# Performance work log

Hardware: AMD Instinct MI355X
Metric: run time of the kernel (lower is better)

The kernel has to match this reference:

```python
import jax, jax.numpy as jnp
import numpy as np

B, S, D_IN = 2, 2048, 1024
H, DH = 16, 64          # num_heads, hidden_size (per-head dim)
D_MODEL = H * DH        # 1024
D_OUT = DH * 8          # 512


def setup_inputs() -> dict:
    key = jax.random.key(0)
    ks = jax.random.split(key, 9)
    s_in = 1.0 / np.sqrt(D_IN)
    s_md = 1.0 / np.sqrt(D_MODEL)
    return {
        "x": jax.random.normal(ks[0], (B, S, D_IN), dtype=jnp.float32),
        "Wq": jax.random.uniform(ks[1], (D_IN, D_MODEL), jnp.float32, -s_in, s_in),
        "bq": jax.random.uniform(ks[2], (D_MODEL,), jnp.float32, -s_in, s_in),
        "Wk": jax.random.uniform(ks[3], (D_IN, D_MODEL), jnp.float32, -s_in, s_in),
        "bk": jax.random.uniform(ks[4], (D_MODEL,), jnp.float32, -s_in, s_in),
        "Wv": jax.random.uniform(ks[5], (D_IN, D_MODEL), jnp.float32, -s_in, s_in),
        "bv": jax.random.uniform(ks[6], (D_MODEL,), jnp.float32, -s_in, s_in),
        "Wo": jax.random.uniform(ks[7], (D_MODEL, D_OUT), jnp.float32, -s_md, s_md),
        "bo": jax.random.uniform(ks[8], (D_OUT,), jnp.float32, -s_md, s_md),
    }


def reference(x, Wq, bq, Wk, bk, Wv, bv, Wo, bo):
    b, s, _ = x.shape
    # QKV projections -> [B, H, S, DH]
    def proj(W, bias):
        y = jnp.einsum("bsd,de->bse", x, W) + bias
        return y.reshape(b, s, H, DH).transpose(0, 2, 1, 3)
    Q, K, V = proj(Wq, bq), proj(Wk, bk), proj(Wv, bv)
    scores = jnp.einsum("bhqd,bhkd->bhqk", Q, K) / jnp.sqrt(jnp.float32(DH))
    weights = jax.nn.softmax(scores, axis=-1)
    attn = jnp.einsum("bhqk,bhkd->bhqd", weights, V)  # [B, H, S, DH]
    attn = attn.transpose(0, 2, 1, 3).reshape(b, s, H * DH)
    return jnp.einsum("bsd,de->bse", attn, Wo) + bo
```

## Files before the change

kernel.cpp:

```cpp
#include <hip/hip_runtime.h>

typedef __attribute__((ext_vector_type(8))) __bf16 bf16x8;
typedef __attribute__((ext_vector_type(4))) __bf16 bf16x4;
typedef __attribute__((ext_vector_type(4))) float f32x4;

#define MFMA16x16x32(A, B, C) __builtin_amdgcn_mfma_f32_16x16x32_bf16(A, B, C, 0, 0, 0)

__device__ __forceinline__ unsigned short f2bf(float f) {
    unsigned int u = __float_as_uint(f);
    u += 0x7fffu + ((u >> 16) & 1u);
    return (unsigned short)(u >> 16);
}

__device__ __forceinline__ unsigned cvtpk_bf16(float lo, float hi) {
    unsigned r;
    asm("v_cvt_pk_bf16_f32 %0, %1, %2" : "=v"(r) : "v"(lo), "v"(hi));
    return r;
}

__device__ __forceinline__ float exp2_hw(float x) {
    float r;
    asm("v_exp_f32 %0, %1" : "=v"(r) : "v"(x));
    return r;
}

__device__ __forceinline__ void gload16(const void* src, void* lds) {
    __builtin_amdgcn_global_load_lds(
        (const __attribute__((address_space(1))) unsigned int*)src,
        (__attribute__((address_space(3))) unsigned int*)lds,
        16, 0, 0);
}

__global__ __launch_bounds__(256) void cvt_x_kernel(const float* __restrict__ x,
                                                    unsigned short* __restrict__ xb) {
    const int i = (blockIdx.x * 256 + threadIdx.x) * 4;
    const float4 v = *(const float4*)(x + i);
    ushort4 o;
    o.x = f2bf(v.x); o.y = f2bf(v.y); o.z = f2bf(v.z); o.w = f2bf(v.w);
    *(ushort4*)(xb + i) = o;
}

__global__ __launch_bounds__(256) void tr_w_kernel(const float* __restrict__ W,
                                                   unsigned short* __restrict__ Wt, int N) {
    __shared__ float tile[32][33];
    const int k0 = blockIdx.x * 32;
    const int n0 = blockIdx.y * 32;
    const int tx = threadIdx.x, ty = threadIdx.y;
#pragma unroll
    for (int i = 0; i < 4; ++i)
        tile[ty + 8 * i][tx] = W[(size_t)(k0 + ty + 8 * i) * N + n0 + tx];
    __syncthreads();
#pragma unroll
    for (int i = 0; i < 4; ++i)
        Wt[(size_t)(n0 + ty + 8 * i) * 1024 + k0 + tx] = f2bf(tile[tx][ty + 8 * i]);
}

__global__ __launch_bounds__(256) void tr_v_kernel(const unsigned short* __restrict__ Vb,
                                                   unsigned short* __restrict__ Vt) {
    __shared__ unsigned short tile[32][33];
    const int bh = blockIdx.z;
    const int s0 = blockIdx.x * 32;
    const int d0 = blockIdx.y * 32;
    const int tx = threadIdx.x, ty = threadIdx.y;
#pragma unroll
    for (int i = 0; i < 4; ++i)
        tile[ty + 8 * i][tx] = Vb[((size_t)bh * 2048 + s0 + ty + 8 * i) * 64 + d0 + tx];
    __syncthreads();
#pragma unroll
    for (int i = 0; i < 4; ++i)
        Vt[((size_t)bh * 64 + d0 + ty + 8 * i) * 2048 + s0 + tx] = tile[tx][ty + 8 * i];
}

__global__ __launch_bounds__(256, 2) void gemm_qkv_kernel(
    const unsigned short* __restrict__ xb,
    const unsigned short* __restrict__ Wqt,
    const unsigned short* __restrict__ Wkt,
    const unsigned short* __restrict__ Wvt,
    const float* __restrict__ bq, const float* __restrict__ bk, const float* __restrict__ bv,
    unsigned short* __restrict__ Qb, unsigned short* __restrict__ Kb, unsigned short* __restrict__ Vb)
{
    __shared__ unsigned short sA[2][128 * 32];
    __shared__ unsigned short sB[2][128 * 32];

    const int tid  = threadIdx.x;
    const int lane = tid & 63;
    const int w    = tid >> 6;
    const int wm   = w >> 1, wn = w & 1;
    const int li   = lane & 15, gg = lane >> 4;
    const int m0   = blockIdx.y * 128;
    const int which = blockIdx.x >> 3;
    const int nloc0 = (blockIdx.x & 7) * 128;

    const unsigned short* Wt = (which == 0) ? Wqt : ((which == 1) ? Wkt : Wvt);
    const float* bias        = (which == 0) ? bq  : ((which == 1) ? bk  : bv);
    unsigned short* dst      = (which == 0) ? Qb  : ((which == 1) ? Kb  : Vb);
    const float osc          = (which == 0) ? 0.18033688011112042f : 1.0f;

    const int srow = lane >> 2;
    const int schk = lane & 3;

    f32x4 acc[4][4];
#pragma unroll
    for (int i = 0; i < 4; ++i)
#pragma unroll
        for (int j = 0; j < 4; ++j)
            acc[i][j] = (f32x4){0.f, 0.f, 0.f, 0.f};

    int aoff[4], boff[4];
#pragma unroll
    for (int f = 0; f < 4; ++f) {
        const int ra = wm * 64 + f * 16 + li;
        aoff[f] = ra * 32 + ((gg ^ ((ra >> 1) & 3)) * 8);
        const int rb = wn * 64 + f * 16 + li;
        boff[f] = rb * 32 + ((gg ^ ((rb >> 1) & 3)) * 8);
    }

#pragma unroll
    for (int j = 0; j < 2; ++j) {
        const int rl = (w * 2 + j) * 16 + srow;
        const int c  = schk ^ ((rl >> 1) & 3);
        gload16(xb + (size_t)(m0 + rl) * 1024 + c * 8,   sA[0] + (w * 2 + j) * 512);
        gload16(Wt + (size_t)(nloc0 + rl) * 1024 + c * 8, sB[0] + (w * 2 + j) * 512);
    }
    __syncthreads();

    for (int kt = 0; kt < 32; ++kt) {
        const int cur = kt & 1;
        if (kt < 31) {
            const int k1 = (kt + 1) * 32;
#pragma unroll
            for (int j = 0; j < 2; ++j) {
                const int rl = (w * 2 + j) * 16 + srow;
                const int c  = schk ^ ((rl >> 1) & 3);
                gload16(xb + (size_t)(m0 + rl) * 1024 + k1 + c * 8,   sA[cur ^ 1] + (w * 2 + j) * 512);
                gload16(Wt + (size_t)(nloc0 + rl) * 1024 + k1 + c * 8, sB[cur ^ 1] + (w * 2 + j) * 512);
            }
        }
        bf16x8 av[4], bw[4];
#pragma unroll
        for (int f = 0; f < 4; ++f) av[f] = *(const bf16x8*)(sA[cur] + aoff[f]);
#pragma unroll
        for (int f = 0; f < 4; ++f) bw[f] = *(const bf16x8*)(sB[cur] + boff[f]);
#pragma unroll
        for (int mf = 0; mf < 4; ++mf)
#pragma unroll
            for (int nf = 0; nf < 4; ++nf)
                acc[mf][nf] = MFMA16x16x32(av[mf], bw[nf], acc[mf][nf]);
        __syncthreads();
    }

#pragma unroll
    for (int nf = 0; nf < 4; ++nf) {
        const int nl = nloc0 + wn * 64 + nf * 16 + li;
        const float bi = bias[nl];
        const int h = nl >> 6, d = nl & 63;
#pragma unroll
        for (int mf = 0; mf < 4; ++mf) {
#pragma unroll
            for (int r = 0; r < 4; ++r) {
                const int m = m0 + wm * 64 + mf * 16 + gg * 4 + r;
                const int b = m >> 11, s = m & 2047;
                dst[(((size_t)(b * 16 + h)) * 2048 + s) * 64 + d] = f2bf((acc[mf][nf][r] + bi) * osc);
            }
        }
    }
}

__global__ __launch_bounds__(512, 4) void attn_kernel(
    const unsigned short* __restrict__ Qb,
    const unsigned short* __restrict__ Kb,
    const unsigned short* __restrict__ Vt,
    unsigned short* __restrict__ Ob)
{
    __shared__ unsigned short sK[2][64 * 64];
    __shared__ unsigned short sV[2][64 * 64];
    __shared__ unsigned short sP[8][16 * 64];

    const int tid  = threadIdx.x;
    const int lane = tid & 63;
    const int w    = tid >> 6;
    const int li   = lane & 15, gg = lane >> 4;

    const int L  = blockIdx.y * 16 + blockIdx.x;
    const int v  = (L & 7) * 64 + (L >> 3);
    const int bh = v >> 4;
    const int q0 = (v & 15) * 128 + w * 16;

    const int slot = w * 64 + lane;
    const int srow = slot >> 3;
    const int schk = (slot & 7) ^ (srow & 7);

    char* const sPw = (char*)sP[w];
    const int swz = (li & 7) << 4;

    bf16x8 qf[2];
#pragma unroll
    for (int kk = 0; kk < 2; ++kk) {
        const int q = q0 + li;
        const int d = kk * 32 + gg * 8;
        qf[kk] = *(const bf16x8*)(Qb + ((size_t)bh * 2048 + q) * 64 + d);
    }

    f32x4 acc[4];
#pragma unroll
    for (int df = 0; df < 4; ++df) acc[df] = (f32x4){0.f, 0.f, 0.f, 0.f};
    float m_s = -1e30f, l_s = 0.f;

    gload16(Kb + ((size_t)bh * 2048 + srow) * 64 + schk * 8, sK[0] + slot * 8);
    gload16(Vt + ((size_t)bh * 64 + srow) * 2048 + schk * 8, sV[0] + slot * 8);
    __syncthreads();

    for (int t = 0; t < 32; ++t) {
        const int cur = t & 1;
        if (t < 31) {
            gload16(Kb + ((size_t)bh * 2048 + (t + 1) * 64 + srow) * 64 + schk * 8,
                    sK[cur ^ 1] + slot * 8);
            gload16(Vt + ((size_t)bh * 64 + srow) * 2048 + (t + 1) * 64 + schk * 8,
                    sV[cur ^ 1] + slot * 8);
        }

        bf16x8 kf[4][2];
#pragma unroll
        for (int nf = 0; nf < 4; ++nf)
#pragma unroll
            for (int kk = 0; kk < 2; ++kk) {
                const int n = nf * 16 + li;
                const int ch = kk * 4 + gg;
                kf[nf][kk] = *(const bf16x8*)(sK[cur] + n * 64 + ((ch ^ (n & 7)) * 8));
            }
        f32x4 st[4];
#pragma unroll
        for (int nf = 0; nf < 4; ++nf) {
            st[nf] = (f32x4){0.f, 0.f, 0.f, 0.f};
            st[nf] = MFMA16x16x32(kf[nf][0], qf[0], st[nf]);
            st[nf] = MFMA16x16x32(kf[nf][1], qf[1], st[nf]);
        }

        float t0 = fmaxf(fmaxf(st[0][0], st[0][1]), fmaxf(st[0][2], st[0][3]));
        float t1 = fmaxf(fmaxf(st[1][0], st[1][1]), fmaxf(st[1][2], st[1][3]));
        float t2 = fmaxf(fmaxf(st[2][0], st[2][1]), fmaxf(st[2][2], st[2][3]));
        float t3 = fmaxf(fmaxf(st[3][0], st[3][1]), fmaxf(st[3][2], st[3][3]));
        float tm = fmaxf(fmaxf(t0, t1), fmaxf(t2, t3));
        tm = fmaxf(tm, __shfl_xor(tm, 16, 64));
        tm = fmaxf(tm, __shfl_xor(tm, 32, 64));

        if (!__all(tm - m_s <= 8.0f)) {
            const float mnew = fmaxf(m_s, tm);
            const float alpha = exp2_hw(m_s - mnew);
            m_s = mnew;
            l_s *= alpha;
            float al[4];
#pragma unroll
            for (int r = 0; r < 4; ++r) al[r] = __shfl(alpha, gg * 4 + r, 64);
#pragma unroll
            for (int df = 0; df < 4; ++df)
#pragma unroll
                for (int r = 0; r < 4; ++r)
                    acc[df][r] *= al[r];
        }

        float rs = 0.f;
#pragma unroll
        for (int nf = 0; nf < 4; ++nf)
#pragma unroll
            for (int r = 0; r < 4; ++r) {
                const float p = exp2_hw(st[nf][r] - m_s);
                st[nf][r] = p;
                rs += p;
            }
        rs += __shfl_xor(rs, 16, 64);
        rs += __shfl_xor(rs, 32, 64);
        l_s += rs;

#pragma unroll
        for (int nf = 0; nf < 4; ++nf) {
            uint2 pv;
            pv.x = cvtpk_bf16(st[nf][0], st[nf][1]);
            pv.y = cvtpk_bf16(st[nf][2], st[nf][3]);
            const int byte = (li * 128 + nf * 32 + gg * 8) ^ swz;
            *(uint2*)(sPw + byte) = pv;
        }

        bf16x8 pf[2];
#pragma unroll
        for (int kk = 0; kk < 2; ++kk) {
            const int byte = (li * 128 + kk * 64 + gg * 16) ^ swz;
            pf[kk] = *(const bf16x8*)(sPw + byte);
        }
        bf16x8 vf[4][2];
#pragma unroll
        for (int df = 0; df < 4; ++df)
#pragma unroll
            for (int kk = 0; kk < 2; ++kk) {
                const int n = df * 16 + li;
                const int ch = kk * 4 + gg;
                vf[df][kk] = *(const bf16x8*)(sV[cur] + n * 64 + ((ch ^ (n & 7)) * 8));
            }
#pragma unroll
        for (int df = 0; df < 4; ++df) {
            acc[df] = MFMA16x16x32(pf[0], vf[df][0], acc[df]);
            acc[df] = MFMA16x16x32(pf[1], vf[df][1], acc[df]);
        }
        __syncthreads();
    }

    const int b = bh >> 4, h = bh & 15;
#pragma unroll
    for (int r = 0; r < 4; ++r) {
        const float lbc = __shfl(l_s, gg * 4 + r, 64);
        const float rl = 1.0f / lbc;
        const int q = q0 + gg * 4 + r;
#pragma unroll
        for (int df = 0; df < 4; ++df) {
            const int d = df * 16 + li;
            Ob[(((size_t)b * 2048 + q) * 16 + h) * 64 + d] = f2bf(acc[df][r] * rl);
        }
    }
}

__global__ __launch_bounds__(256, 2) void gemm_out_kernel(
    const unsigned short* __restrict__ attn,
    const unsigned short* __restrict__ Wot,
    const float* __restrict__ bo,
    float* __restrict__ out)
{
    __shared__ unsigned short sA[2][64 * 32];
    __shared__ unsigned short sB[2][128 * 32];

    const int tid  = threadIdx.x;
    const int lane = tid & 63;
    const int w    = tid >> 6;
    const int wm   = w >> 1, wn = w & 1;
    const int li   = lane & 15, gg = lane >> 4;
    const int m0   = blockIdx.y * 64;
    const int n0   = blockIdx.x * 128;

    const int arow = tid >> 2;
    const int acol = tid & 3;

    f32x4 acc[2][4];
#pragma unroll
    for (int i = 0; i < 2; ++i)
#pragma unroll
        for (int j = 0; j < 4; ++j)
            acc[i][j] = (f32x4){0.f, 0.f, 0.f, 0.f};

    int aoff[2], boff[4];
#pragma unroll
    for (int f = 0; f < 2; ++f) {
        const int ra = wm * 32 + f * 16 + li;
        aoff[f] = ra * 32 + ((gg ^ ((ra >> 1) & 3)) * 8);
    }
#pragma unroll
    for (int f = 0; f < 4; ++f) {
        const int rb = wn * 64 + f * 16 + li;
        boff[f] = rb * 32 + ((gg ^ ((rb >> 1) & 3)) * 8);
    }

    {
        const int ca = acol ^ ((arow >> 1) & 3);
        gload16(attn + (size_t)(m0 + arow) * 1024 + ca * 8, sA[0] + tid * 8);
#pragma unroll
        for (int jj = 0; jj < 2; ++jj) {
            const int rb = jj * 64 + arow;
            const int cb = acol ^ ((rb >> 1) & 3);
            gload16(Wot + (size_t)(n0 + rb) * 1024 + cb * 8, sB[0] + (jj * 256 + tid) * 8);
        }
    }
    __syncthreads();

    for (int kt = 0; kt < 32; ++kt) {
        const int cur = kt & 1;
        if (kt < 31) {
            const int k1 = (kt + 1) * 32;
            const int ca = acol ^ ((arow >> 1) & 3);
            gload16(attn + (size_t)(m0 + arow) * 1024 + k1 + ca * 8, sA[cur ^ 1] + tid * 8);
#pragma unroll
            for (int jj = 0; jj < 2; ++jj) {
                const int rb = jj * 64 + arow;
                const int cb = acol ^ ((rb >> 1) & 3);
                gload16(Wot + (size_t)(n0 + rb) * 1024 + k1 + cb * 8, sB[cur ^ 1] + (jj * 256 + tid) * 8);
            }
        }
        bf16x8 av[2], bw[4];
#pragma unroll
        for (int f = 0; f < 2; ++f) av[f] = *(const bf16x8*)(sA[cur] + aoff[f]);
#pragma unroll
        for (int f = 0; f < 4; ++f) bw[f] = *(const bf16x8*)(sB[cur] + boff[f]);
#pragma unroll
        for (int mf = 0; mf < 2; ++mf)
#pragma unroll
            for (int nf = 0; nf < 4; ++nf)
                acc[mf][nf] = MFMA16x16x32(av[mf], bw[nf], acc[mf][nf]);
        __syncthreads();
    }

#pragma unroll
    for (int nf = 0; nf < 4; ++nf) {
        const int n = n0 + wn * 64 + nf * 16 + li;
        const float bi = bo[n];
#pragma unroll
        for (int mf = 0; mf < 2; ++mf) {
#pragma unroll
            for (int r = 0; r < 4; ++r) {
                const int m = m0 + wm * 32 + mf * 16 + gg * 4 + r;
                out[(size_t)m * 512 + n] = acc[mf][nf][r] + bi;
            }
        }
    }
}

extern "C" void kernel_launch(void* const* d_in, const int* in_sizes, int n_in,
                              void* d_out, int out_size, void* d_ws, size_t ws_size,
                              hipStream_t stream) {
    const float* x  = (const float*)d_in[0];
    const float* Wq = (const float*)d_in[1];
    const float* bq = (const float*)d_in[2];
    const float* Wk = (const float*)d_in[3];
    const float* bk = (const float*)d_in[4];
    const float* Wv = (const float*)d_in[5];
    const float* bv = (const float*)d_in[6];
    const float* Wo = (const float*)d_in[7];
    const float* bo = (const float*)d_in[8];
    float* out = (float*)d_out;

    unsigned short* ws  = (unsigned short*)d_ws;
    unsigned short* xb  = ws;
    unsigned short* Wqt = xb  + 4194304;
    unsigned short* Wkt = Wqt + 1048576;
    unsigned short* Wvt = Wkt + 1048576;
    unsigned short* Wot = Wvt + 1048576;
    unsigned short* Qb  = Wot + 524288;
    unsigned short* Kb  = Qb  + 4194304;
    unsigned short* Vb  = Kb  + 4194304;
    unsigned short* Vt  = Vb  + 4194304;
    unsigned short* attnb = Vt + 4194304;

    cvt_x_kernel<<<dim3(4096), dim3(256), 0, stream>>>(x, xb);
    tr_w_kernel<<<dim3(32, 32), dim3(32, 8), 0, stream>>>(Wq, Wqt, 1024);
    tr_w_kernel<<<dim3(32, 32), dim3(32, 8), 0, stream>>>(Wk, Wkt, 1024);
    tr_w_kernel<<<dim3(32, 32), dim3(32, 8), 0, stream>>>(Wv, Wvt, 1024);
    tr_w_kernel<<<dim3(32, 16), dim3(32, 8), 0, stream>>>(Wo, Wot, 512);
    gemm_qkv_kernel<<<dim3(24, 32), dim3(256), 0, stream>>>(xb, Wqt, Wkt, Wvt,
                                                            bq, bk, bv, Qb, Kb, Vb);
    tr_v_kernel<<<dim3(64, 2, 32), dim3(32, 8), 0, stream>>>(Vb, Vt);
    attn_kernel<<<dim3(16, 32), dim3(512), 0, stream>>>(Qb, Kb, Vt, attnb);
    gemm_out_kernel<<<dim3(4, 64), dim3(256), 0, stream>>>(attnb, Wot, bo, out);
}
```

Baseline: 129.5 us.

## Process two query sub-tiles per wave in attention to reuse K/V fragments

The attention kernel now runs 4 waves of 256 threads per block instead of 8, and each wave handles 32 query rows as two 16-row sub-tiles. K and V fragments read from shared memory are reused across both sub-tiles, which halves the LDS reads of K/V per unit of MFMA work, and each thread issues twice as many global-to-LDS loads. The cost is more registers per thread (double accumulators, scores and Q fragments), a lower occupancy bound, and a combined rescale test shared by both sub-tiles.

```diff
diff --git a/kernel.cpp b/kernel.cpp
--- a/kernel.cpp
+++ b/kernel.cpp
@@ -166,7 +166,7 @@
     }
 }
 
-__global__ __launch_bounds__(512, 4) void attn_kernel(
+__global__ __launch_bounds__(256, 2) void attn_kernel(
     const unsigned short* __restrict__ Qb,
     const unsigned short* __restrict__ Kb,
     const unsigned short* __restrict__ Vt,
@@ -174,7 +174,7 @@
 {
     __shared__ unsigned short sK[2][64 * 64];
     __shared__ unsigned short sV[2][64 * 64];
-    __shared__ unsigned short sP[8][16 * 64];
+    __shared__ unsigned short sP[4][32 * 64];
 
     const int tid  = threadIdx.x;
     const int lane = tid & 63;
@@ -184,39 +184,54 @@
     const int L  = blockIdx.y * 16 + blockIdx.x;
     const int v  = (L & 7) * 64 + (L >> 3);
     const int bh = v >> 4;
-    const int q0 = (v & 15) * 128 + w * 16;
-
-    const int slot = w * 64 + lane;
-    const int srow = slot >> 3;
-    const int schk = (slot & 7) ^ (srow & 7);
+    const int q0 = (v & 15) * 128 + w * 32;
+
+    const int slot0 = w * 64 + lane;
+    const int srow0 = slot0 >> 3;
+    const int sch0  = (slot0 & 7) ^ (srow0 & 7);
 
     char* const sPw = (char*)sP[w];
     const int swz = (li & 7) << 4;
 
-    bf16x8 qf[2];
-#pragma unroll
-    for (int kk = 0; kk < 2; ++kk) {
-        const int q = q0 + li;
-        const int d = kk * 32 + gg * 8;
-        qf[kk] = *(const bf16x8*)(Qb + ((size_t)bh * 2048 + q) * 64 + d);
-    }
-
-    f32x4 acc[4];
-#pragma unroll
-    for (int df = 0; df < 4; ++df) acc[df] = (f32x4){0.f, 0.f, 0.f, 0.f};
-    float m_s = -1e30f, l_s = 0.f;
-
-    gload16(Kb + ((size_t)bh * 2048 + srow) * 64 + schk * 8, sK[0] + slot * 8);
-    gload16(Vt + ((size_t)bh * 64 + srow) * 2048 + schk * 8, sV[0] + slot * 8);
+    bf16x8 qf[2][2];
+#pragma unroll
+    for (int mq = 0; mq < 2; ++mq)
+#pragma unroll
+        for (int kk = 0; kk < 2; ++kk) {
+            const int q = q0 + mq * 16 + li;
+            const int d = kk * 32 + gg * 8;
+            qf[mq][kk] = *(const bf16x8*)(Qb + ((size_t)bh * 2048 + q) * 64 + d);
+        }
+
+    f32x4 acc[2][4];
+    float m_s[2], l_s[2];
+#pragma unroll
+    for (int mq = 0; mq < 2; ++mq) {
+#pragma unroll
+        for (int df = 0; df < 4; ++df) acc[mq][df] = (f32x4){0.f, 0.f, 0.f, 0.f};
+        m_s[mq] = -1e30f; l_s[mq] = 0.f;
+    }
+
+    {
+        const unsigned short* Kp = Kb + ((size_t)bh * 2048) * 64;
+        const unsigned short* Vp = Vt + ((size_t)bh * 64) * 2048;
+        gload16(Kp + (size_t)srow0 * 64 + sch0 * 8,        sK[0] + slot0 * 8);
+        gload16(Kp + (size_t)(srow0 + 32) * 64 + sch0 * 8, sK[0] + slot0 * 8 + 2048);
+        gload16(Vp + (size_t)srow0 * 2048 + sch0 * 8,        sV[0] + slot0 * 8);
+        gload16(Vp + (size_t)(srow0 + 32) * 2048 + sch0 * 8, sV[0] + slot0 * 8 + 2048);
+    }
     __syncthreads();
 
     for (int t = 0; t < 32; ++t) {
         const int cur = t & 1;
         if (t < 31) {
-            gload16(Kb + ((size_t)bh * 2048 + (t + 1) * 64 + srow) * 64 + schk * 8,
-                    sK[cur ^ 1] + slot * 8);
-            gload16(Vt + ((size_t)bh * 64 + srow) * 2048 + (t + 1) * 64 + schk * 8,
-                    sV[cur ^ 1] + slot * 8);
+            const int toff = (t + 1) * 64;
+            const unsigned short* Kp = Kb + ((size_t)bh * 2048 + toff) * 64;
+            const unsigned short* Vp = Vt + ((size_t)bh * 64) * 2048 + toff;
+            gload16(Kp + (size_t)srow0 * 64 + sch0 * 8,        sK[cur ^ 1] + slot0 * 8);
+            gload16(Kp + (size_t)(srow0 + 32) * 64 + sch0 * 8, sK[cur ^ 1] + slot0 * 8 + 2048);
+            gload16(Vp + (size_t)srow0 * 2048 + sch0 * 8,        sV[cur ^ 1] + slot0 * 8);
+            gload16(Vp + (size_t)(srow0 + 32) * 2048 + sch0 * 8, sV[cur ^ 1] + slot0 * 8 + 2048);
         }
 
         bf16x8 kf[4][2];
@@ -228,65 +243,81 @@
                 const int ch = kk * 4 + gg;
                 kf[nf][kk] = *(const bf16x8*)(sK[cur] + n * 64 + ((ch ^ (n & 7)) * 8));
             }
-        f32x4 st[4];
-#pragma unroll
-        for (int nf = 0; nf < 4; ++nf) {
-            st[nf] = (f32x4){0.f, 0.f, 0.f, 0.f};
-            st[nf] = MFMA16x16x32(kf[nf][0], qf[0], st[nf]);
-            st[nf] = MFMA16x16x32(kf[nf][1], qf[1], st[nf]);
-        }
-
-        float t0 = fmaxf(fmaxf(st[0][0], st[0][1]), fmaxf(st[0][2], st[0][3]));
-        float t1 = fmaxf(fmaxf(st[1][0], st[1][1]), fmaxf(st[1][2], st[1][3]));
-        float t2 = fmaxf(fmaxf(st[2][0], st[2][1]), fmaxf(st[2][2], st[2][3]));
-        float t3 = fmaxf(fmaxf(st[3][0], st[3][1]), fmaxf(st[3][2], st[3][3]));
-        float tm = fmaxf(fmaxf(t0, t1), fmaxf(t2, t3));
-        tm = fmaxf(tm, __shfl_xor(tm, 16, 64));
-        tm = fmaxf(tm, __shfl_xor(tm, 32, 64));
-
-        if (!__all(tm - m_s <= 8.0f)) {
-            const float mnew = fmaxf(m_s, tm);
-            const float alpha = exp2_hw(m_s - mnew);
-            m_s = mnew;
-            l_s *= alpha;
-            float al[4];
-#pragma unroll
-            for (int r = 0; r < 4; ++r) al[r] = __shfl(alpha, gg * 4 + r, 64);
-#pragma unroll
-            for (int df = 0; df < 4; ++df)
-#pragma unroll
-                for (int r = 0; r < 4; ++r)
-                    acc[df][r] *= al[r];
-        }
-
-        float rs = 0.f;
-#pragma unroll
-        for (int nf = 0; nf < 4; ++nf)
-#pragma unroll
-            for (int r = 0; r < 4; ++r) {
-                const float p = exp2_hw(st[nf][r] - m_s);
-                st[nf][r] = p;
-                rs += p;
-            }
-        rs += __shfl_xor(rs, 16, 64);
-        rs += __shfl_xor(rs, 32, 64);
-        l_s += rs;
-
-#pragma unroll
-        for (int nf = 0; nf < 4; ++nf) {
-            uint2 pv;
-            pv.x = cvtpk_bf16(st[nf][0], st[nf][1]);
-            pv.y = cvtpk_bf16(st[nf][2], st[nf][3]);
-            const int byte = (li * 128 + nf * 32 + gg * 8) ^ swz;
-            *(uint2*)(sPw + byte) = pv;
-        }
-
-        bf16x8 pf[2];
-#pragma unroll
-        for (int kk = 0; kk < 2; ++kk) {
-            const int byte = (li * 128 + kk * 64 + gg * 16) ^ swz;
-            pf[kk] = *(const bf16x8*)(sPw + byte);
-        }
+        f32x4 st[2][4];
+#pragma unroll
+        for (int mq = 0; mq < 2; ++mq)
+#pragma unroll
+            for (int nf = 0; nf < 4; ++nf) {
+                st[mq][nf] = (f32x4){0.f, 0.f, 0.f, 0.f};
+                st[mq][nf] = MFMA16x16x32(kf[nf][0], qf[mq][0], st[mq][nf]);
+                st[mq][nf] = MFMA16x16x32(kf[nf][1], qf[mq][1], st[mq][nf]);
+            }
+
+        float tmv[2];
+#pragma unroll
+        for (int mq = 0; mq < 2; ++mq) {
+            float t0 = fmaxf(fmaxf(st[mq][0][0], st[mq][0][1]), fmaxf(st[mq][0][2], st[mq][0][3]));
+            float t1 = fmaxf(fmaxf(st[mq][1][0], st[mq][1][1]), fmaxf(st[mq][1][2], st[mq][1][3]));
+            float t2 = fmaxf(fmaxf(st[mq][2][0], st[mq][2][1]), fmaxf(st[mq][2][2], st[mq][2][3]));
+            float t3 = fmaxf(fmaxf(st[mq][3][0], st[mq][3][1]), fmaxf(st[mq][3][2], st[mq][3][3]));
+            float tm = fmaxf(fmaxf(t0, t1), fmaxf(t2, t3));
+            tm = fmaxf(tm, __shfl_xor(tm, 16, 64));
+            tm = fmaxf(tm, __shfl_xor(tm, 32, 64));
+            tmv[mq] = tm;
+        }
+
+        const float need = fmaxf(tmv[0] - m_s[0], tmv[1] - m_s[1]);
+        if (!__all(need <= 8.0f)) {
+#pragma unroll
+            for (int mq = 0; mq < 2; ++mq) {
+                const float mnew = fmaxf(m_s[mq], tmv[mq]);
+                const float alpha = exp2_hw(m_s[mq] - mnew);
+                m_s[mq] = mnew;
+                l_s[mq] *= alpha;
+                float al[4];
+#pragma unroll
+                for (int r = 0; r < 4; ++r) al[r] = __shfl(alpha, gg * 4 + r, 64);
+#pragma unroll
+                for (int df = 0; df < 4; ++df)
+#pragma unroll
+                    for (int r = 0; r < 4; ++r)
+                        acc[mq][df][r] *= al[r];
+            }
+        }
+
+#pragma unroll
+        for (int mq = 0; mq < 2; ++mq) {
+            float rs = 0.f;
+#pragma unroll
+            for (int nf = 0; nf < 4; ++nf)
+#pragma unroll
+                for (int r = 0; r < 4; ++r) {
+                    const float p = exp2_hw(st[mq][nf][r] - m_s[mq]);
+                    st[mq][nf][r] = p;
+                    rs += p;
+                }
+            rs += __shfl_xor(rs, 16, 64);
+            rs += __shfl_xor(rs, 32, 64);
+            l_s[mq] += rs;
+
+#pragma unroll
+            for (int nf = 0; nf < 4; ++nf) {
+                uint2 pv;
+                pv.x = cvtpk_bf16(st[mq][nf][0], st[mq][nf][1]);
+                pv.y = cvtpk_bf16(st[mq][nf][2], st[mq][nf][3]);
+                const int byte = ((mq * 16 + li) * 128 + nf * 32 + gg * 8) ^ swz;
+                *(uint2*)(sPw + byte) = pv;
+            }
+        }
+
+        bf16x8 pf[2][2];
+#pragma unroll
+        for (int mq = 0; mq < 2; ++mq)
+#pragma unroll
+            for (int kk = 0; kk < 2; ++kk) {
+                const int byte = ((mq * 16 + li) * 128 + kk * 64 + gg * 16) ^ swz;
+                pf[mq][kk] = *(const bf16x8*)(sPw + byte);
+            }
         bf16x8 vf[4][2];
 #pragma unroll
         for (int df = 0; df < 4; ++df)
@@ -297,25 +328,29 @@
                 vf[df][kk] = *(const bf16x8*)(sV[cur] + n * 64 + ((ch ^ (n & 7)) * 8));
             }
 #pragma unroll
-        for (int df = 0; df < 4; ++df) {
-            acc[df] = MFMA16x16x32(pf[0], vf[df][0], acc[df]);
-            acc[df] = MFMA16x16x32(pf[1], vf[df][1], acc[df]);
-        }
+        for (int mq = 0; mq < 2; ++mq)
+#pragma unroll
+            for (int df = 0; df < 4; ++df) {
+                acc[mq][df] = MFMA16x16x32(pf[mq][0], vf[df][0], acc[mq][df]);
+                acc[mq][df] = MFMA16x16x32(pf[mq][1], vf[df][1], acc[mq][df]);
+            }
         __syncthreads();
     }
 
     const int b = bh >> 4, h = bh & 15;
 #pragma unroll
-    for (int r = 0; r < 4; ++r) {
-        const float lbc = __shfl(l_s, gg * 4 + r, 64);
-        const float rl = 1.0f / lbc;
-        const int q = q0 + gg * 4 + r;
-#pragma unroll
-        for (int df = 0; df < 4; ++df) {
-            const int d = df * 16 + li;
-            Ob[(((size_t)b * 2048 + q) * 16 + h) * 64 + d] = f2bf(acc[df][r] * rl);
-        }
-    }
+    for (int mq = 0; mq < 2; ++mq)
+#pragma unroll
+        for (int r = 0; r < 4; ++r) {
+            const float lbc = __shfl(l_s[mq], gg * 4 + r, 64);
+            const float rl = 1.0f / lbc;
+            const int q = q0 + mq * 16 + gg * 4 + r;
+#pragma unroll
+            for (int df = 0; df < 4; ++df) {
+                const int d = df * 16 + li;
+                Ob[(((size_t)b * 2048 + q) * 16 + h) * 64 + d] = f2bf(acc[mq][df][r] * rl);
+            }
+        }
 }
 
 __global__ __launch_bounds__(256, 2) void gemm_out_kernel(
@@ -444,6 +479,6 @@
     gemm_qkv_kernel<<<dim3(24, 32), dim3(256), 0, stream>>>(xb, Wqt, Wkt, Wvt,
                                                             bq, bk, bv, Qb, Kb, Vb);
     tr_v_kernel<<<dim3(64, 2, 32), dim3(32, 8), 0, stream>>>(Vb, Vt);
-    attn_kernel<<<dim3(16, 32), dim3(512), 0, stream>>>(Qb, Kb, Vt, attnb);
+    attn_kernel<<<dim3(16, 32), dim3(256), 0, stream>>>(Qb, Kb, Vt, attnb);
     gemm_out_kernel<<<dim3(4, 64), dim3(256), 0, stream>>>(attnb, Wot, bo, out);
 }
```

Measured after the change: 133.4 us. 3.0% more time.

## Fuse V transpose into QKV GEMM epilogue and remap block order

Applied to the files above, without the earlier changes.

The QKV projection GEMM now writes V directly in transposed [bh, d, s] layout using 4-element vector stores, which removes the separate tr_v_kernel launch and its intermediate V buffer round trip. The block index is remapped so consecutive launched blocks are spread across the output tiles, a swizzle that may change L2 locality or XCD distribution. The launch bound is raised from 2 to 3 blocks per SIMD, which may force register pressure or spills in exchange for occupancy.

```diff
diff --git a/kernel.cpp b/kernel.cpp
--- a/kernel.cpp
+++ b/kernel.cpp
@@ -55,29 +55,13 @@
         Wt[(size_t)(n0 + ty + 8 * i) * 1024 + k0 + tx] = f2bf(tile[tx][ty + 8 * i]);
 }
 
-__global__ __launch_bounds__(256) void tr_v_kernel(const unsigned short* __restrict__ Vb,
-                                                   unsigned short* __restrict__ Vt) {
-    __shared__ unsigned short tile[32][33];
-    const int bh = blockIdx.z;
-    const int s0 = blockIdx.x * 32;
-    const int d0 = blockIdx.y * 32;
-    const int tx = threadIdx.x, ty = threadIdx.y;
-#pragma unroll
-    for (int i = 0; i < 4; ++i)
-        tile[ty + 8 * i][tx] = Vb[((size_t)bh * 2048 + s0 + ty + 8 * i) * 64 + d0 + tx];
-    __syncthreads();
-#pragma unroll
-    for (int i = 0; i < 4; ++i)
-        Vt[((size_t)bh * 64 + d0 + ty + 8 * i) * 2048 + s0 + tx] = tile[tx][ty + 8 * i];
-}
-
-__global__ __launch_bounds__(256, 2) void gemm_qkv_kernel(
+__global__ __launch_bounds__(256, 3) void gemm_qkv_kernel(
     const unsigned short* __restrict__ xb,
     const unsigned short* __restrict__ Wqt,
     const unsigned short* __restrict__ Wkt,
     const unsigned short* __restrict__ Wvt,
     const float* __restrict__ bq, const float* __restrict__ bk, const float* __restrict__ bv,
-    unsigned short* __restrict__ Qb, unsigned short* __restrict__ Kb, unsigned short* __restrict__ Vb)
+    unsigned short* __restrict__ Qb, unsigned short* __restrict__ Kb, unsigned short* __restrict__ Vt)
 {
     __shared__ unsigned short sA[2][128 * 32];
     __shared__ unsigned short sB[2][128 * 32];
@@ -87,13 +71,17 @@
     const int w    = tid >> 6;
     const int wm   = w >> 1, wn = w & 1;
     const int li   = lane & 15, gg = lane >> 4;
-    const int m0   = blockIdx.y * 128;
-    const int which = blockIdx.x >> 3;
-    const int nloc0 = (blockIdx.x & 7) * 128;
+
+    const int L  = blockIdx.y * 24 + blockIdx.x;
+    const int v  = (L & 7) * 96 + (L >> 3);
+    const int vx = v >> 5;
+    const int vy = v & 31;
+    const int m0    = vy * 128;
+    const int which = vx >> 3;
+    const int nloc0 = (vx & 7) * 128;
 
     const unsigned short* Wt = (which == 0) ? Wqt : ((which == 1) ? Wkt : Wvt);
     const float* bias        = (which == 0) ? bq  : ((which == 1) ? bk  : bv);
-    unsigned short* dst      = (which == 0) ? Qb  : ((which == 1) ? Kb  : Vb);
     const float osc          = (which == 0) ? 0.18033688011112042f : 1.0f;
 
     const int srow = lane >> 2;
@@ -149,18 +137,39 @@
         __syncthreads();
     }
 
-#pragma unroll
-    for (int nf = 0; nf < 4; ++nf) {
-        const int nl = nloc0 + wn * 64 + nf * 16 + li;
-        const float bi = bias[nl];
-        const int h = nl >> 6, d = nl & 63;
-#pragma unroll
-        for (int mf = 0; mf < 4; ++mf) {
-#pragma unroll
-            for (int r = 0; r < 4; ++r) {
-                const int m = m0 + wm * 64 + mf * 16 + gg * 4 + r;
-                const int b = m >> 11, s = m & 2047;
-                dst[(((size_t)(b * 16 + h)) * 2048 + s) * 64 + d] = f2bf((acc[mf][nf][r] + bi) * osc);
+    if (which == 2) {
+#pragma unroll
+        for (int nf = 0; nf < 4; ++nf) {
+            const int nl = nloc0 + wn * 64 + nf * 16 + li;
+            const float bi = bias[nl];
+            const int h = nl >> 6, d = nl & 63;
+#pragma unroll
+            for (int mf = 0; mf < 4; ++mf) {
+                const int m = m0 + wm * 64 + mf * 16 + gg * 4;
+                const int b = m >> 11, s0 = m & 2047;
+                ushort4 o;
+                o.x = f2bf(acc[mf][nf][0] + bi);
+                o.y = f2bf(acc[mf][nf][1] + bi);
+                o.z = f2bf(acc[mf][nf][2] + bi);
+                o.w = f2bf(acc[mf][nf][3] + bi);
+                *(ushort4*)(Vt + (((size_t)(b * 16 + h)) * 64 + d) * 2048 + s0) = o;
+            }
+        }
+    } else {
+        unsigned short* dst = (which == 0) ? Qb : Kb;
+#pragma unroll
+        for (int nf = 0; nf < 4; ++nf) {
+            const int nl = nloc0 + wn * 64 + nf * 16 + li;
+            const float bi = bias[nl];
+            const int h = nl >> 6, d = nl & 63;
+#pragma unroll
+            for (int mf = 0; mf < 4; ++mf) {
+#pragma unroll
+                for (int r = 0; r < 4; ++r) {
+                    const int m = m0 + wm * 64 + mf * 16 + gg * 4 + r;
+                    const int b = m >> 11, s = m & 2047;
+                    dst[(((size_t)(b * 16 + h)) * 2048 + s) * 64 + d] = f2bf((acc[mf][nf][r] + bi) * osc);
+                }
             }
         }
     }
@@ -432,8 +441,7 @@
     unsigned short* Wot = Wvt + 1048576;
     unsigned short* Qb  = Wot + 524288;
     unsigned short* Kb  = Qb  + 4194304;
-    unsigned short* Vb  = Kb  + 4194304;
-    unsigned short* Vt  = Vb  + 4194304;
+    unsigned short* Vt  = Kb  + 4194304;
     unsigned short* attnb = Vt + 4194304;
 
     cvt_x_kernel<<<dim3(4096), dim3(256), 0, stream>>>(x, xb);
@@ -442,8 +450,7 @@
     tr_w_kernel<<<dim3(32, 32), dim3(32, 8), 0, stream>>>(Wv, Wvt, 1024);
     tr_w_kernel<<<dim3(32, 16), dim3(32, 8), 0, stream>>>(Wo, Wot, 512);
     gemm_qkv_kernel<<<dim3(24, 32), dim3(256), 0, stream>>>(xb, Wqt, Wkt, Wvt,
-                                                            bq, bk, bv, Qb, Kb, Vb);
-    tr_v_kernel<<<dim3(64, 2, 32), dim3(32, 8), 0, stream>>>(Vb, Vt);
+                                                            bq, bk, bv, Qb, Kb, Vt);
     attn_kernel<<<dim3(16, 32), dim3(512), 0, stream>>>(Qb, Kb, Vt, attnb);
     gemm_out_kernel<<<dim3(4, 64), dim3(256), 0, stream>>>(attnb, Wot, bo, out);
 }
```

Result: faster. 124.6 us (-3.8%).
